# Kernel tuning notes

Hardware: AMD Instinct MI355X
Metric: run time of the kernel (lower is better)

Reference implementation:

```python
import jax, jax.numpy as jnp
import numpy as np

D_MODEL = 256
NHEAD = 8
D_FF = 2 * D_MODEL
N_LAYERS = 4
LAYER_NAMES = ("self", "cross", "self", "cross")
EPS_ATTN = 1e-6
EPS_LN = 1e-5


def pos_encoding(x):
    # LoFTR-style 2D sinusoidal positional encoding, x: [N, C, H, W]
    n, c, h, w = x.shape
    d4 = c // 4
    # exp(arange(0, c//2, 2) * (-log(1e4) / (c//2)))
    div = jnp.exp(jnp.arange(d4, dtype=jnp.float32) * 2.0 * (-np.log(10000.0) / (c // 2)))
    xs = jnp.arange(w, dtype=jnp.float32)[None, None, :]   # [1,1,W]
    ys = jnp.arange(h, dtype=jnp.float32)[None, :, None]   # [1,H,1]
    dv = div[:, None, None]                                 # [d4,1,1]
    sx = jnp.broadcast_to(jnp.sin(xs * dv), (d4, h, w))
    cx = jnp.broadcast_to(jnp.cos(xs * dv), (d4, h, w))
    sy = jnp.broadcast_to(jnp.sin(ys * dv), (d4, h, w))
    cy = jnp.broadcast_to(jnp.cos(ys * dv), (d4, h, w))
    pe = jnp.stack([sx, cx, sy, cy], axis=1).reshape(c, h, w)  # channel order pe[0::4]=sin_x,...
    return x + pe[None]


def linear_attention(q, k, v):
    # q: [N,L,H,d], k/v: [N,S,H,d]
    Q = jax.nn.elu(q) + 1.0
    K = jax.nn.elu(k) + 1.0
    KV = jnp.einsum('nshd,nshm->nhmd', K, v)                 # [N,H,d,d]
    Z = 1.0 / (jnp.einsum('nlhd,nhd->nlh', Q, K.sum(axis=1)) + EPS_ATTN)
    return jnp.einsum('nlhd,nhmd,nlh->nlhm', Q, KV, Z)       # [N,L,H,d]


def layer_norm(x, g, b):
    m = jnp.mean(x, axis=-1, keepdims=True)
    v = jnp.mean(jnp.square(x - m), axis=-1, keepdims=True)
    return (x - m) / jnp.sqrt(v + EPS_LN) * g + b


def encoder_layer(x, src, p):
    N, L, _ = x.shape
    q = (x @ p['Wq'] + p['bq']).reshape(N, L, NHEAD, -1)
    S = src.shape[1]
    k = (src @ p['Wk'] + p['bk']).reshape(N, S, NHEAD, -1)
    v = (src @ p['Wv'] + p['bv']).reshape(N, S, NHEAD, -1)
    attn = linear_attention(q, k, v).reshape(N, L, -1) @ p['Wo'] + p['bo']
    x = layer_norm(x + attn, p['g1'], p['be1'])
    y = jax.nn.relu(x @ p['W1'] + p['b1']) @ p['W2'] + p['b2']
    return layer_norm(x + y, p['g2'], p['be2'])


def _params_at(i, Wq, bq, Wk, bk, Wv, bv, Wo, bo, W1, b1, W2, b2, g1, be1, g2, be2):
    return dict(Wq=Wq[i], bq=bq[i], Wk=Wk[i], bk=bk[i], Wv=Wv[i], bv=bv[i],
                Wo=Wo[i], bo=bo[i], W1=W1[i], b1=b1[i], W2=W2[i], b2=b2[i],
                g1=g1[i], be1=be1[i], g2=g2[i], be2=be2[i])


def setup_inputs() -> dict:
    key = jax.random.key(0)
    ks = jax.random.split(key, 16)
    N, C, H, W = 4, D_MODEL, 64, 64
    d, dff, Ln = D_MODEL, D_FF, N_LAYERS
    s = 1.0 / np.sqrt(d)
    sf = 1.0 / np.sqrt(dff)
    return {
        'ref_feature': jax.random.normal(ks[0], (N, C, H, W), jnp.float32),
        'src_feature': jax.random.normal(ks[1], (N, C, H, W), jnp.float32),
        'Wq': jax.random.normal(ks[2], (Ln, d, d), jnp.float32) * s,
        'bq': jnp.zeros((Ln, d), jnp.float32),
        'Wk': jax.random.normal(ks[3], (Ln, d, d), jnp.float32) * s,
        'bk': jnp.zeros((Ln, d), jnp.float32),
        'Wv': jax.random.normal(ks[4], (Ln, d, d), jnp.float32) * s,
        'bv': jnp.zeros((Ln, d), jnp.float32),
        'Wo': jax.random.normal(ks[5], (Ln, d, d), jnp.float32) * s,
        'bo': jnp.zeros((Ln, d), jnp.float32),
        'W1': jax.random.normal(ks[6], (Ln, d, dff), jnp.float32) * s,
        'b1': jnp.zeros((Ln, dff), jnp.float32),
        'W2': jax.random.normal(ks[7], (Ln, dff, d), jnp.float32) * sf,
        'b2': jnp.zeros((Ln, d), jnp.float32),
        'g1': jnp.ones((Ln, d), jnp.float32),
        'be1': jnp.zeros((Ln, d), jnp.float32),
        'g2': jnp.ones((Ln, d), jnp.float32),
        'be2': jnp.zeros((Ln, d), jnp.float32),
    }


def reference(ref_feature, src_feature, Wq, bq, Wk, bk, Wv, bv, Wo, bo,
              W1, b1, W2, b2, g1, be1, g2, be2):
    # FMT.forward(feat='cross')
    N, C, H, W = ref_feature.shape
    f0 = pos_encoding(ref_feature).transpose(0, 2, 3, 1).reshape(N, H * W, C)
    f1 = pos_encoding(src_feature).transpose(0, 2, 3, 1).reshape(N, H * W, C)
    p1 = jnp.concatenate([f0, f1], axis=0)   # [2N, L, C]
    p2 = jnp.concatenate([f1, f0], axis=0)
    for i, name in enumerate(LAYER_NAMES):
        p = _params_at(i, Wq, bq, Wk, bk, Wv, bv, Wo, bo, W1, b1, W2, b2, g1, be1, g2, be2)
        src = p1 if name == 'self' else p2
        p1 = encoder_layer(p1, src, p)
    out = p1.reshape(2 * N, H, W, C).transpose(0, 3, 1, 2)  # [2N, C, H, W]
    return out
```

## Files before the change

kernel.cpp:

```cpp
#include <hip/hip_runtime.h>
#include <hip/hip_bf16.h>

typedef __bf16 bf16;
typedef __attribute__((ext_vector_type(8))) __bf16 bf16x8;
typedef __attribute__((ext_vector_type(4))) __bf16 bf16x4;
typedef __attribute__((ext_vector_type(4))) float f32x4;

__device__ __forceinline__ bf16 f2bf(float f) { return (bf16)f; }

__device__ __forceinline__ void async_cp16(const void* g, void* l) {
    __builtin_amdgcn_global_load_lds(
        (const __attribute__((address_space(1))) unsigned int*)g,
        (__attribute__((address_space(3))) unsigned int*)l, 16, 0, 0);
}

__device__ __forceinline__ float pe_val(int c, int t) {
    int h = t >> 6, w = t & 63;
    int i = c >> 2, j = c & 3;
    float div = expf(-0.14391156831212787f * (float)i);
    float arg = ((j < 2) ? (float)w : (float)h) * div;
    return (j & 1) ? cosf(arg) : sinf(arg);
}

__global__ __launch_bounds__(1024) void encode_kernel(const float* __restrict__ ref,
                                                      const float* __restrict__ src,
                                                      bf16* __restrict__ Xb,
                                                      bf16* __restrict__ P2b) {
    __shared__ float tile[32][33];
    int n = blockIdx.z >> 1, sel = blockIdx.z & 1;
    const float* f = sel ? src : ref;
    int t = blockIdx.x * 32 + threadIdx.x;
    int c = blockIdx.y * 32 + threadIdx.y;
    float v = f[((size_t)n * 256 + c) * 4096 + t] + pe_val(c, t);
    tile[threadIdx.y][threadIdx.x] = v;
    __syncthreads();
    int tt = blockIdx.x * 32 + threadIdx.y;
    int cc = blockIdx.y * 32 + threadIdx.x;
    float o = tile[threadIdx.x][threadIdx.y];
    int bx = sel ? 4 + n : n;
    int bp = sel ? n : 4 + n;
    Xb [((size_t)bx * 4096 + tt) * 256 + cc] = f2bf(o);
    P2b[((size_t)bp * 4096 + tt) * 256 + cc] = f2bf(o);
}

__global__ __launch_bounds__(1024) void wt_conv(const float* __restrict__ Wq, const float* __restrict__ Wk,
                                                const float* __restrict__ Wv, const float* __restrict__ Wo,
                                                const float* __restrict__ W1, const float* __restrict__ W2,
                                                bf16* __restrict__ Wt) {
    __shared__ float t[32][33];
    int z = blockIdx.z, L = z / 6, m = z - L * 6;
    const float* src; int K, N, doff;
    if      (m == 0) { src = Wq + L * 65536;  K = 256; N = 256; doff = 0; }
    else if (m == 1) { src = Wk + L * 65536;  K = 256; N = 256; doff = 65536; }
    else if (m == 2) { src = Wv + L * 65536;  K = 256; N = 256; doff = 131072; }
    else if (m == 3) { src = Wo + L * 65536;  K = 256; N = 256; doff = 196608; }
    else if (m == 4) { src = W1 + L * 131072; K = 256; N = 512; doff = 262144; }
    else             { src = W2 + L * 131072; K = 512; N = 256; doff = 393216; }
    int n0 = blockIdx.x * 32, k0 = blockIdx.y * 32;
    if (n0 >= N || k0 >= K) return;
    t[threadIdx.y][threadIdx.x] = src[(size_t)(k0 + threadIdx.y) * N + n0 + threadIdx.x];
    __syncthreads();
    bf16* dst = Wt + (size_t)L * 524288 + doff;
    dst[(size_t)(n0 + threadIdx.y) * K + k0 + threadIdx.x] = f2bf(t[threadIdx.x][threadIdx.y]);
}

__global__ __launch_bounds__(256) void gemm_qkv(const bf16* __restrict__ Aq,
                                                const bf16* __restrict__ Akv,
                                                const bf16* __restrict__ Wt,
                                                const float* __restrict__ bq,
                                                const float* __restrict__ bk,
                                                const float* __restrict__ bv,
                                                bf16* __restrict__ Q,
                                                bf16* __restrict__ Ko,
                                                bf16* __restrict__ V) {
    __shared__ bf16 Als[128 * 64];
    __shared__ bf16 Bls[128 * 64];
    int tid = threadIdx.x;
    int wave = tid >> 6, lane = tid & 63;
    int bm = blockIdx.y * 128, bn = blockIdx.x * 128;
    int wm = (wave >> 1) * 64, wn = (wave & 1) * 64;
    int l15 = lane & 15, g = lane >> 4;
    const int K = 256;

    int seg = bn >> 8, cloc = bn & 255;
    const bf16* A = seg == 0 ? Aq : Akv;
    const float* bias = seg == 0 ? bq : (seg == 1 ? bk : bv);
    bf16* Out = seg == 0 ? Q : (seg == 1 ? Ko : V);
    bool do_elu = seg < 2;

    f32x4 acc[4][4] = {};

    for (int k0 = 0; k0 < K; k0 += 64) {
#pragma unroll
        for (int r = 0; r < 4; ++r) {
            int Lc = r * 256 + tid;
            int row = Lc >> 3, cs = Lc & 7;
            int gc = cs ^ (row & 7);
            async_cp16(A  + (size_t)(bm + row) * K + k0 + gc * 8, &Als[Lc * 8]);
            async_cp16(Wt + (size_t)(bn + row) * K + k0 + gc * 8, &Bls[Lc * 8]);
        }
        __syncthreads();
#pragma unroll
        for (int ks = 0; ks < 2; ++ks) {
            bf16x8 af[4], bfr[4];
#pragma unroll
            for (int i = 0; i < 4; ++i) {
                int row = wm + i * 16 + l15;
                int c = ks * 4 + g;
                af[i] = *(bf16x8*)&Als[row * 64 + ((c ^ (row & 7)) * 8)];
            }
#pragma unroll
            for (int j = 0; j < 4; ++j) {
                int row = wn + j * 16 + l15;
                int c = ks * 4 + g;
                bfr[j] = *(bf16x8*)&Bls[row * 64 + ((c ^ (row & 7)) * 8)];
            }
#pragma unroll
            for (int i = 0; i < 4; ++i)
#pragma unroll
                for (int j = 0; j < 4; ++j)
                    acc[i][j] = __builtin_amdgcn_mfma_f32_16x16x32_bf16(af[i], bfr[j], acc[i][j], 0, 0, 0);
        }
        __syncthreads();
    }

    int r4 = (lane >> 4) * 4;
#pragma unroll
    for (int i = 0; i < 4; ++i) {
#pragma unroll
        for (int j = 0; j < 4; ++j) {
            int cj = cloc + wn + j * 16 + l15;
            float bvv = bias[cj];
#pragma unroll
            for (int r = 0; r < 4; ++r) {
                int row = bm + wm + i * 16 + r4 + r;
                float v = acc[i][j][r] + bvv;
                if (do_elu) v = v > 0.f ? v + 1.f : expf(v);
                Out[(size_t)row * 256 + cj] = f2bf(v);
            }
        }
    }
}

template <int RELU>
__global__ __launch_bounds__(256) void gemm_mfma(const bf16* __restrict__ A,
                                                 const bf16* __restrict__ Wt,
                                                 const float* __restrict__ bias,
                                                 bf16* __restrict__ C,
                                                 int N, int K) {
    __shared__ bf16 Als[128 * 64];
    __shared__ bf16 Bls[128 * 64];
    int tid = threadIdx.x;
    int wave = tid >> 6, lane = tid & 63;
    int bm = blockIdx.y * 128, bn = blockIdx.x * 128;
    int wm = (wave >> 1) * 64, wn = (wave & 1) * 64;
    int l15 = lane & 15, g = lane >> 4;

    f32x4 acc[4][4] = {};

    for (int k0 = 0; k0 < K; k0 += 64) {
#pragma unroll
        for (int r = 0; r < 4; ++r) {
            int Lc = r * 256 + tid;
            int row = Lc >> 3, cs = Lc & 7;
            int gc = cs ^ (row & 7);
            async_cp16(A  + (size_t)(bm + row) * K + k0 + gc * 8, &Als[Lc * 8]);
            async_cp16(Wt + (size_t)(bn + row) * K + k0 + gc * 8, &Bls[Lc * 8]);
        }
        __syncthreads();
#pragma unroll
        for (int ks = 0; ks < 2; ++ks) {
            bf16x8 af[4], bfr[4];
#pragma unroll
            for (int i = 0; i < 4; ++i) {
                int row = wm + i * 16 + l15;
                int c = ks * 4 + g;
                af[i] = *(bf16x8*)&Als[row * 64 + ((c ^ (row & 7)) * 8)];
            }
#pragma unroll
            for (int j = 0; j < 4; ++j) {
                int row = wn + j * 16 + l15;
                int c = ks * 4 + g;
                bfr[j] = *(bf16x8*)&Bls[row * 64 + ((c ^ (row & 7)) * 8)];
            }
#pragma unroll
            for (int i = 0; i < 4; ++i)
#pragma unroll
                for (int j = 0; j < 4; ++j)
                    acc[i][j] = __builtin_amdgcn_mfma_f32_16x16x32_bf16(af[i], bfr[j], acc[i][j], 0, 0, 0);
        }
        __syncthreads();
    }

    int r4 = (lane >> 4) * 4;
#pragma unroll
    for (int i = 0; i < 4; ++i) {
#pragma unroll
        for (int j = 0; j < 4; ++j) {
            int col = bn + wn + j * 16 + l15;
            float bvv = bias[col];
#pragma unroll
            for (int r = 0; r < 4; ++r) {
                int row = bm + wm + i * 16 + r4 + r;
                float v = acc[i][j][r] + bvv;
                if (RELU) v = fmaxf(v, 0.f);
                C[(size_t)row * N + col] = f2bf(v);
            }
        }
    }
}

__global__ __launch_bounds__(512) void gemm_ln(const bf16* __restrict__ A,
                                               const bf16* __restrict__ Wt,
                                               const float* __restrict__ bias,
                                               bf16* __restrict__ Xb,
                                               const float* __restrict__ g,
                                               const float* __restrict__ b,
                                               int K) {
    __shared__ __align__(16) char smem[128 * 260 * 2];
    bf16* Als = (bf16*)smem;
    bf16* Bls = (bf16*)(smem + 16384);
    bf16* Cls = (bf16*)smem;

    int tid = threadIdx.x;
    int wave = tid >> 6, lane = tid & 63;
    int bm = blockIdx.x * 128;
    int wm = (wave >> 2) * 64, wn = (wave & 3) * 64;
    int l15 = lane & 15, gg = lane >> 4;

    f32x4 acc[4][4] = {};

    for (int k0 = 0; k0 < K; k0 += 64) {
#pragma unroll
        for (int r = 0; r < 2; ++r) {
            int Lc = r * 512 + tid;
            int row = Lc >> 3, cs = Lc & 7;
            int gc = cs ^ (row & 7);
            async_cp16(A + (size_t)(bm + row) * K + k0 + gc * 8, &Als[Lc * 8]);
        }
#pragma unroll
        for (int r = 0; r < 4; ++r) {
            int Lc = r * 512 + tid;
            int row = Lc >> 3, cs = Lc & 7;
            int gc = cs ^ (row & 7);
            async_cp16(Wt + (size_t)row * K + k0 + gc * 8, &Bls[Lc * 8]);
        }
        __syncthreads();
#pragma unroll
        for (int ks = 0; ks < 2; ++ks) {
            bf16x8 af[4], bfr[4];
#pragma unroll
            for (int i = 0; i < 4; ++i) {
                int row = wm + i * 16 + l15;
                int c = ks * 4 + gg;
                af[i] = *(bf16x8*)&Als[row * 64 + ((c ^ (row & 7)) * 8)];
            }
#pragma unroll
            for (int j = 0; j < 4; ++j) {
                int row = wn + j * 16 + l15;
                int c = ks * 4 + gg;
                bfr[j] = *(bf16x8*)&Bls[row * 64 + ((c ^ (row & 7)) * 8)];
            }
#pragma unroll
            for (int i = 0; i < 4; ++i)
#pragma unroll
                for (int j = 0; j < 4; ++j)
                    acc[i][j] = __builtin_amdgcn_mfma_f32_16x16x32_bf16(af[i], bfr[j], acc[i][j], 0, 0, 0);
        }
        __syncthreads();
    }

    int r4 = (lane >> 4) * 4;
#pragma unroll
    for (int j = 0; j < 4; ++j) {
        int col = wn + j * 16 + l15;
        float bvv = bias[col];
#pragma unroll
        for (int i = 0; i < 4; ++i)
#pragma unroll
            for (int r = 0; r < 4; ++r)
                Cls[(wm + i * 16 + r4 + r) * 260 + col] = f2bf(acc[i][j][r] + bvv);
    }
    __syncthreads();

    int c4 = lane * 4;
    float4 gw = *(const float4*)&g[c4];
    float4 bw = *(const float4*)&b[c4];
#pragma unroll 2
    for (int rw = 0; rw < 16; ++rw) {
        int row = wave * 16 + rw;
        size_t gidx = (size_t)(bm + row) * 256 + c4;
        bf16x4 xb = *(const bf16x4*)(Xb + gidx);
        bf16x4 cb = *(const bf16x4*)&Cls[row * 260 + c4];
        float4 v;
        v.x = (float)xb[0] + (float)cb[0];
        v.y = (float)xb[1] + (float)cb[1];
        v.z = (float)xb[2] + (float)cb[2];
        v.w = (float)xb[3] + (float)cb[3];
        float s  = v.x + v.y + v.z + v.w;
        float sq = v.x * v.x + v.y * v.y + v.z * v.z + v.w * v.w;
#pragma unroll
        for (int off = 32; off > 0; off >>= 1) {
            s  += __shfl_xor(s,  off);
            sq += __shfl_xor(sq, off);
        }
        float mean = s * (1.f / 256.f);
        float var  = sq * (1.f / 256.f) - mean * mean;
        float rstd = rsqrtf(var + 1e-5f);
        bf16x4 ob;
        ob[0] = f2bf((v.x - mean) * rstd * gw.x + bw.x);
        ob[1] = f2bf((v.y - mean) * rstd * gw.y + bw.y);
        ob[2] = f2bf((v.z - mean) * rstd * gw.z + bw.z);
        ob[3] = f2bf((v.w - mean) * rstd * gw.w + bw.w);
        *(bf16x4*)(Xb + gidx) = ob;
    }
}

__global__ __launch_bounds__(256) void kv_prep_part(const bf16* __restrict__ Kb,
                                                    const bf16* __restrict__ Vb,
                                                    float* __restrict__ Pkv,
                                                    float* __restrict__ Pks) {
    __shared__ float Ks[128][32];
    __shared__ float Vs[128][32];
    int sp = blockIdx.x;
    int nh = blockIdx.y;
    int n = nh >> 3, h = nh & 7;
    int tid = threadIdx.x;
    int wave = tid >> 6, lane = tid & 63;
    int mg = lane >> 3;
    int dg = lane & 7;
    size_t base = ((size_t)n * 4096 + sp * 128) * 256 + h * 32;

#pragma unroll
    for (int p = 0; p < 2; ++p) {
        int r = p * 64 + (tid >> 2);
        int c = (tid & 3) * 8;
        bf16x8 k8 = *(const bf16x8*)(Kb + base + (size_t)r * 256 + c);
        bf16x8 v8 = *(const bf16x8*)(Vb + base + (size_t)r * 256 + c);
#pragma unroll
        for (int u = 0; u < 8; ++u) { Ks[r][c + u] = (float)k8[u]; Vs[r][c + u] = (float)v8[u]; }
    }
    __syncthreads();

    float acc[4][4] = {};
    float ks4[4] = {};
    int s0 = wave * 32;
    for (int s = s0; s < s0 + 32; ++s) {
        float4 kq = *(float4*)&Ks[s][dg * 4];
        float4 vq = *(float4*)&Vs[s][mg * 4];
        ks4[0] += kq.x; ks4[1] += kq.y; ks4[2] += kq.z; ks4[3] += kq.w;
        acc[0][0] += vq.x * kq.x; acc[0][1] += vq.x * kq.y; acc[0][2] += vq.x * kq.z; acc[0][3] += vq.x * kq.w;
        acc[1][0] += vq.y * kq.x; acc[1][1] += vq.y * kq.y; acc[1][2] += vq.y * kq.z; acc[1][3] += vq.y * kq.w;
        acc[2][0] += vq.z * kq.x; acc[2][1] += vq.z * kq.y; acc[2][2] += vq.z * kq.z; acc[2][3] += vq.z * kq.w;
        acc[3][0] += vq.w * kq.x; acc[3][1] += vq.w * kq.y; acc[3][2] += vq.w * kq.z; acc[3][3] += vq.w * kq.w;
    }
    __syncthreads();

    float* R  = &Ks[0][0];
    float* RS = &Vs[0][0];
#pragma unroll
    for (int mi = 0; mi < 4; ++mi)
#pragma unroll
        for (int dj = 0; dj < 4; ++dj)
            R[wave * 1024 + (mg * 4 + mi) * 32 + dg * 4 + dj] = acc[mi][dj];
    if (mg == 0)
#pragma unroll
        for (int dj = 0; dj < 4; ++dj) RS[wave * 32 + dg * 4 + dj] = ks4[dj];
    __syncthreads();

    int e = tid * 4;
    float4 o0 = *(float4*)&R[e];
    float4 o1 = *(float4*)&R[1024 + e];
    float4 o2 = *(float4*)&R[2048 + e];
    float4 o3 = *(float4*)&R[3072 + e];
    float4 o = make_float4(o0.x + o1.x + o2.x + o3.x, o0.y + o1.y + o2.y + o3.y,
                           o0.z + o1.z + o2.z + o3.z, o0.w + o1.w + o2.w + o3.w);
    *(float4*)&Pkv[((size_t)nh * 32 + sp) * 1024 + e] = o;
    if (tid < 32)
        Pks[((size_t)nh * 32 + sp) * 32 + tid] = RS[tid] + RS[32 + tid] + RS[64 + tid] + RS[96 + tid];
}

__global__ __launch_bounds__(64) void kv_reduce(const float* __restrict__ Pkv,
                                                const float* __restrict__ Pks,
                                                float* __restrict__ KV,
                                                float* __restrict__ Ksum) {
    int nh = blockIdx.x;
    int q = blockIdx.y;
    int e = (q * 64 + threadIdx.x) * 4;
    float4 s = make_float4(0.f, 0.f, 0.f, 0.f);
    for (int sp = 0; sp < 32; ++sp) {
        float4 p = *(const float4*)&Pkv[((size_t)nh * 32 + sp) * 1024 + e];
        s.x += p.x; s.y += p.y; s.z += p.z; s.w += p.w;
    }
    *(float4*)&KV[(size_t)nh * 1024 + e] = s;
    if (q == 0 && threadIdx.x < 32) {
        float ss = 0.f;
        for (int sp = 0; sp < 32; ++sp) ss += Pks[((size_t)nh * 32 + sp) * 32 + threadIdx.x];
        Ksum[nh * 32 + threadIdx.x] = ss;
    }
}

__global__ __launch_bounds__(256) void attn_apply(const bf16* __restrict__ Qb,
                                                  const float* __restrict__ KV,
                                                  const float* __restrict__ Ksum,
                                                  bf16* __restrict__ B) {
    __shared__ float Qs[32][260];
    __shared__ float Zs[32][8];
    int bx = blockIdx.x;
    int n = bx >> 7;
    int tok0 = (bx & 127) << 5;
    int tid = threadIdx.x;

    const bf16* qsrc = Qb + ((size_t)(n * 4096 + tok0)) * 256;
#pragma unroll
    for (int kk = 0; kk < 4; ++kk) {
        int e8 = tid + kk * 256;
        bf16x8 v = *(const bf16x8*)(qsrc + (size_t)e8 * 8);
        int t = e8 >> 5, c8 = e8 & 31;
#pragma unroll
        for (int u = 0; u < 8; ++u) Qs[t][c8 * 8 + u] = (float)v[u];
    }

    int h = tid >> 5, m = tid & 31;
    float kvr[32];
    const float* kvp = KV + (size_t)(n * 8 + h) * 1024 + m * 32;
#pragma unroll
    for (int c = 0; c < 8; ++c) *(float4*)&kvr[c * 4] = *(const float4*)(kvp + c * 4);
    __syncthreads();

    {
        int tz = tid >> 3, hz = tid & 7;
        const float* ksp = Ksum + n * 256 + hz * 32;
        float z = 0.f;
#pragma unroll
        for (int c = 0; c < 8; ++c) {
            float4 q = *(float4*)&Qs[tz][hz * 32 + c * 4];
            float4 k = *(const float4*)(ksp + c * 4);
            z += q.x * k.x + q.y * k.y + q.z * k.z + q.w * k.w;
        }
        Zs[tz][hz] = 1.f / (z + 1e-6f);
    }
    __syncthreads();

    bf16* outp = B + ((size_t)(n * 4096 + tok0)) * 256 + tid;
#pragma unroll 2
    for (int t = 0; t < 32; ++t) {
        float acc = 0.f;
#pragma unroll
        for (int c = 0; c < 8; ++c) {
            float4 q = *(float4*)&Qs[t][h * 32 + c * 4];
            acc += q.x * kvr[c * 4 + 0] + q.y * kvr[c * 4 + 1]
                 + q.z * kvr[c * 4 + 2] + q.w * kvr[c * 4 + 3];
        }
        outp[(size_t)t * 256] = f2bf(acc * Zs[t][h]);
    }
}

__global__ __launch_bounds__(1024) void store_kernel(const bf16* __restrict__ Xb,
                                                     float* __restrict__ out) {
    __shared__ float tile[32][33];
    int b = blockIdx.z;
    int t0 = blockIdx.x * 32, c0 = blockIdx.y * 32;
    tile[threadIdx.y][threadIdx.x] =
        (float)Xb[((size_t)b * 4096 + t0 + threadIdx.y) * 256 + c0 + threadIdx.x];
    __syncthreads();
    out[((size_t)b * 256 + c0 + threadIdx.y) * 4096 + t0 + threadIdx.x] =
        tile[threadIdx.x][threadIdx.y];
}

extern "C" void kernel_launch(void* const* d_in, const int* in_sizes, int n_in,
                              void* d_out, int out_size, void* d_ws, size_t ws_size,
                              hipStream_t stream) {
    const float* ref  = (const float*)d_in[0];
    const float* srcf = (const float*)d_in[1];
    const float* Wq = (const float*)d_in[2];
    const float* bq = (const float*)d_in[3];
    const float* Wk = (const float*)d_in[4];
    const float* bk = (const float*)d_in[5];
    const float* Wv = (const float*)d_in[6];
    const float* bv = (const float*)d_in[7];
    const float* Wo = (const float*)d_in[8];
    const float* bo = (const float*)d_in[9];
    const float* W1 = (const float*)d_in[10];
    const float* b1 = (const float*)d_in[11];
    const float* W2 = (const float*)d_in[12];
    const float* b2 = (const float*)d_in[13];
    const float* g1 = (const float*)d_in[14];
    const float* be1 = (const float*)d_in[15];
    const float* g2 = (const float*)d_in[16];
    const float* be2 = (const float*)d_in[17];

    const size_t SZ = (size_t)8 * 4096 * 256;
    float* ws  = (float*)d_ws;
    float* KVb = ws;
    float* Ksb = KVb + 65536;
    float* Pkv = Ksb + 2048;
    float* Pks = Pkv + 2097152;
    bf16*  Wt  = (bf16*)(Pks + 65536);
    bf16*  Xb  = Wt + 2097152;
    bf16*  P2b = Xb + SZ;
    bf16*  Qb  = P2b + SZ;
    bf16*  Kb  = (bf16*)d_out;
    bf16*  Vb  = Kb + SZ;
    bf16*  Bb  = Kb;
    bf16*  Hb  = Kb;

    wt_conv<<<dim3(16, 16, 24), dim3(32, 32), 0, stream>>>(Wq, Wk, Wv, Wo, W1, W2, Wt);
    encode_kernel<<<dim3(128, 8, 8), dim3(32, 32), 0, stream>>>(ref, srcf, Xb, P2b);

    for (int L = 0; L < 4; ++L) {
        const bf16* WtL = Wt + (size_t)L * 524288;
        const bf16* Akv = (L & 1) ? P2b : Xb;
        gemm_qkv<<<dim3(6, 256), 256, 0, stream>>>(Xb, Akv, WtL,
                                                   bq + L * 256, bk + L * 256, bv + L * 256,
                                                   Qb, Kb, Vb);
        kv_prep_part<<<dim3(32, 64), 256, 0, stream>>>(Kb, Vb, Pkv, Pks);
        kv_reduce<<<dim3(64, 4), 64, 0, stream>>>(Pkv, Pks, KVb, Ksb);
        attn_apply<<<1024, 256, 0, stream>>>(Qb, KVb, Ksb, Bb);
        gemm_ln<<<256, 512, 0, stream>>>(Bb, WtL + 196608, bo + L * 256, Xb,
                                         g1 + L * 256, be1 + L * 256, 256);
        gemm_mfma<1><<<dim3(4, 256), 256, 0, stream>>>(Xb, WtL + 262144, b1 + L * 512, Hb, 512, 256);
        gemm_ln<<<256, 512, 0, stream>>>(Hb, WtL + 393216, b2 + L * 256, Xb,
                                         g2 + L * 256, be2 + L * 256, 512);
    }

    store_kernel<<<dim3(128, 8, 8), dim3(32, 32), 0, stream>>>(Xb, (float*)d_out);
}
```

Measured before the change: 691.0 us.

## Fuse attention apply with output projection and LayerNorm into one kernel

Replaces the separate attn_apply kernel and the following gemm_ln (Wo projection + residual + LayerNorm) with a single kernel that computes the attention output for 128 rows into swizzled shared memory and then runs the MFMA projection and LayerNorm from it. This removes the global write and re-read of the attention output buffer and one kernel launch per layer. In exchange, each block uses about 130 KB of LDS and runs the attention phase serially in four 32-token chunks, with only 256 blocks, which lowers occupancy and parallelism for that phase.

```diff
diff --git a/kernel.cpp b/kernel.cpp
--- a/kernel.cpp
+++ b/kernel.cpp
@@ -316,6 +316,161 @@
     }
 }
 
+__global__ __launch_bounds__(512) void attn_oln(const bf16* __restrict__ Qb,
+                                                const float* __restrict__ KV,
+                                                const float* __restrict__ Ksum,
+                                                const bf16* __restrict__ Wt,
+                                                const float* __restrict__ bias,
+                                                bf16* __restrict__ Xb,
+                                                const float* __restrict__ g,
+                                                const float* __restrict__ b) {
+    __shared__ __align__(16) char smem[132096];
+    __shared__ float Zs[32][8];
+    float* Qs  = (float*)smem;
+    bf16*  Wls = (bf16*)smem;
+    bf16*  Cls = (bf16*)smem;
+    bf16*  Bt  = (bf16*)(smem + 66560);
+
+    int tid = threadIdx.x;
+    int r0 = blockIdx.x * 128;
+    int n = r0 >> 12;
+
+    int c = tid & 255, tg = tid >> 8;
+    int h = c >> 5, m = c & 31;
+    float kvr[32];
+    const float* kvp = KV + (size_t)(n * 8 + h) * 1024 + m * 32;
+#pragma unroll
+    for (int q4 = 0; q4 < 8; ++q4) *(float4*)&kvr[q4 * 4] = *(const float4*)(kvp + q4 * 4);
+
+    int col8 = (c >> 3) & 7, elem = c & 7, slice = c >> 6;
+
+    for (int it = 0; it < 4; ++it) {
+        int t0 = it * 32;
+        const bf16* qsrc = Qb + (size_t)(r0 + t0) * 256;
+#pragma unroll
+        for (int kk = 0; kk < 2; ++kk) {
+            int e8 = kk * 512 + tid;
+            bf16x8 v = *(const bf16x8*)(qsrc + (size_t)e8 * 8);
+            int t = e8 >> 5, c8 = e8 & 31;
+#pragma unroll
+            for (int u = 0; u < 8; ++u) Qs[t * 260 + c8 * 8 + u] = (float)v[u];
+        }
+        __syncthreads();
+        if (tid < 256) {
+            int tz = tid >> 3, hz = tid & 7;
+            const float* ksp = Ksum + n * 256 + hz * 32;
+            float z = 0.f;
+#pragma unroll
+            for (int q4 = 0; q4 < 8; ++q4) {
+                float4 qv = *(float4*)&Qs[tz * 260 + hz * 32 + q4 * 4];
+                float4 kq = *(const float4*)(ksp + q4 * 4);
+                z += qv.x * kq.x + qv.y * kq.y + qv.z * kq.z + qv.w * kq.w;
+            }
+            Zs[tz][hz] = 1.f / (z + 1e-6f);
+        }
+        __syncthreads();
+#pragma unroll 2
+        for (int tt = 0; tt < 16; ++tt) {
+            int t = tg * 16 + tt;
+            float acc = 0.f;
+#pragma unroll
+            for (int q4 = 0; q4 < 8; ++q4) {
+                float4 qv = *(float4*)&Qs[t * 260 + h * 32 + q4 * 4];
+                acc += qv.x * kvr[q4 * 4 + 0] + qv.y * kvr[q4 * 4 + 1]
+                     + qv.z * kvr[q4 * 4 + 2] + qv.w * kvr[q4 * 4 + 3];
+            }
+            int row = t0 + t;
+            Bt[slice * 8192 + row * 64 + ((col8 ^ (row & 7)) * 8) + elem] =
+                f2bf(acc * Zs[t][h]);
+        }
+        __syncthreads();
+    }
+
+    int wave = tid >> 6, lane = tid & 63;
+    int wm = (wave >> 2) * 64, wn = (wave & 3) * 64;
+    int l15 = lane & 15, gg = lane >> 4;
+    f32x4 acc[4][4] = {};
+
+    for (int k0 = 0; k0 < 256; k0 += 64) {
+#pragma unroll
+        for (int r = 0; r < 4; ++r) {
+            int Lc = r * 512 + tid;
+            int row = Lc >> 3, cs = Lc & 7;
+            int gc = cs ^ (row & 7);
+            async_cp16(Wt + (size_t)row * 256 + k0 + gc * 8, &Wls[Lc * 8]);
+        }
+        __syncthreads();
+        const bf16* Asl = Bt + (k0 >> 6) * 8192;
+#pragma unroll
+        for (int ks = 0; ks < 2; ++ks) {
+            bf16x8 af[4], bfr[4];
+#pragma unroll
+            for (int i = 0; i < 4; ++i) {
+                int row = wm + i * 16 + l15;
+                int cc = ks * 4 + gg;
+                af[i] = *(bf16x8*)&Asl[row * 64 + ((cc ^ (row & 7)) * 8)];
+            }
+#pragma unroll
+            for (int j = 0; j < 4; ++j) {
+                int row = wn + j * 16 + l15;
+                int cc = ks * 4 + gg;
+                bfr[j] = *(bf16x8*)&Wls[row * 64 + ((cc ^ (row & 7)) * 8)];
+            }
+#pragma unroll
+            for (int i = 0; i < 4; ++i)
+#pragma unroll
+                for (int j = 0; j < 4; ++j)
+                    acc[i][j] = __builtin_amdgcn_mfma_f32_16x16x32_bf16(af[i], bfr[j], acc[i][j], 0, 0, 0);
+        }
+        __syncthreads();
+    }
+
+    int r4 = (lane >> 4) * 4;
+#pragma unroll
+    for (int j = 0; j < 4; ++j) {
+        int col = wn + j * 16 + l15;
+        float bvv = bias[col];
+#pragma unroll
+        for (int i = 0; i < 4; ++i)
+#pragma unroll
+            for (int r = 0; r < 4; ++r)
+                Cls[(wm + i * 16 + r4 + r) * 260 + col] = f2bf(acc[i][j][r] + bvv);
+    }
+    __syncthreads();
+
+    int c4 = lane * 4;
+    float4 gw = *(const float4*)&g[c4];
+    float4 bw = *(const float4*)&b[c4];
+#pragma unroll 2
+    for (int rw = 0; rw < 16; ++rw) {
+        int row = wave * 16 + rw;
+        size_t gidx = (size_t)(r0 + row) * 256 + c4;
+        bf16x4 xb = *(const bf16x4*)(Xb + gidx);
+        bf16x4 cb = *(const bf16x4*)&Cls[row * 260 + c4];
+        float4 v;
+        v.x = (float)xb[0] + (float)cb[0];
+        v.y = (float)xb[1] + (float)cb[1];
+        v.z = (float)xb[2] + (float)cb[2];
+        v.w = (float)xb[3] + (float)cb[3];
+        float s  = v.x + v.y + v.z + v.w;
+        float sq = v.x * v.x + v.y * v.y + v.z * v.z + v.w * v.w;
+#pragma unroll
+        for (int off = 32; off > 0; off >>= 1) {
+            s  += __shfl_xor(s,  off);
+            sq += __shfl_xor(sq, off);
+        }
+        float mean = s * (1.f / 256.f);
+        float var  = sq * (1.f / 256.f) - mean * mean;
+        float rstd = rsqrtf(var + 1e-5f);
+        bf16x4 ob;
+        ob[0] = f2bf((v.x - mean) * rstd * gw.x + bw.x);
+        ob[1] = f2bf((v.y - mean) * rstd * gw.y + bw.y);
+        ob[2] = f2bf((v.z - mean) * rstd * gw.z + bw.z);
+        ob[3] = f2bf((v.w - mean) * rstd * gw.w + bw.w);
+        *(bf16x4*)(Xb + gidx) = ob;
+    }
+}
+
 __global__ __launch_bounds__(256) void kv_prep_part(const bf16* __restrict__ Kb,
                                                     const bf16* __restrict__ Vb,
                                                     float* __restrict__ Pkv,
@@ -397,62 +552,6 @@
         float ss = 0.f;
         for (int sp = 0; sp < 32; ++sp) ss += Pks[((size_t)nh * 32 + sp) * 32 + threadIdx.x];
         Ksum[nh * 32 + threadIdx.x] = ss;
-    }
-}
-
-__global__ __launch_bounds__(256) void attn_apply(const bf16* __restrict__ Qb,
-                                                  const float* __restrict__ KV,
-                                                  const float* __restrict__ Ksum,
-                                                  bf16* __restrict__ B) {
-    __shared__ float Qs[32][260];
-    __shared__ float Zs[32][8];
-    int bx = blockIdx.x;
-    int n = bx >> 7;
-    int tok0 = (bx & 127) << 5;
-    int tid = threadIdx.x;
-
-    const bf16* qsrc = Qb + ((size_t)(n * 4096 + tok0)) * 256;
-#pragma unroll
-    for (int kk = 0; kk < 4; ++kk) {
-        int e8 = tid + kk * 256;
-        bf16x8 v = *(const bf16x8*)(qsrc + (size_t)e8 * 8);
-        int t = e8 >> 5, c8 = e8 & 31;
-#pragma unroll
-        for (int u = 0; u < 8; ++u) Qs[t][c8 * 8 + u] = (float)v[u];
-    }
-
-    int h = tid >> 5, m = tid & 31;
-    float kvr[32];
-    const float* kvp = KV + (size_t)(n * 8 + h) * 1024 + m * 32;
-#pragma unroll
-    for (int c = 0; c < 8; ++c) *(float4*)&kvr[c * 4] = *(const float4*)(kvp + c * 4);
-    __syncthreads();
-
-    {
-        int tz = tid >> 3, hz = tid & 7;
-        const float* ksp = Ksum + n * 256 + hz * 32;
-        float z = 0.f;
-#pragma unroll
-        for (int c = 0; c < 8; ++c) {
-            float4 q = *(float4*)&Qs[tz][hz * 32 + c * 4];
-            float4 k = *(const float4*)(ksp + c * 4);
-            z += q.x * k.x + q.y * k.y + q.z * k.z + q.w * k.w;
-        }
-        Zs[tz][hz] = 1.f / (z + 1e-6f);
-    }
-    __syncthreads();
-
-    bf16* outp = B + ((size_t)(n * 4096 + tok0)) * 256 + tid;
-#pragma unroll 2
-    for (int t = 0; t < 32; ++t) {
-        float acc = 0.f;
-#pragma unroll
-        for (int c = 0; c < 8; ++c) {
-            float4 q = *(float4*)&Qs[t][h * 32 + c * 4];
-            acc += q.x * kvr[c * 4 + 0] + q.y * kvr[c * 4 + 1]
-                 + q.z * kvr[c * 4 + 2] + q.w * kvr[c * 4 + 3];
-        }
-        outp[(size_t)t * 256] = f2bf(acc * Zs[t][h]);
     }
 }
 
@@ -502,7 +601,6 @@
     bf16*  Qb  = P2b + SZ;
     bf16*  Kb  = (bf16*)d_out;
     bf16*  Vb  = Kb + SZ;
-    bf16*  Bb  = Kb;
     bf16*  Hb  = Kb;
 
     wt_conv<<<dim3(16, 16, 24), dim3(32, 32), 0, stream>>>(Wq, Wk, Wv, Wo, W1, W2, Wt);
@@ -516,9 +614,8 @@
                                                    Qb, Kb, Vb);
         kv_prep_part<<<dim3(32, 64), 256, 0, stream>>>(Kb, Vb, Pkv, Pks);
         kv_reduce<<<dim3(64, 4), 64, 0, stream>>>(Pkv, Pks, KVb, Ksb);
-        attn_apply<<<1024, 256, 0, stream>>>(Qb, KVb, Ksb, Bb);
-        gemm_ln<<<256, 512, 0, stream>>>(Bb, WtL + 196608, bo + L * 256, Xb,
-                                         g1 + L * 256, be1 + L * 256, 256);
+        attn_oln<<<256, 512, 0, stream>>>(Qb, KVb, Ksb, WtL + 196608, bo + L * 256,
+                                          Xb, g1 + L * 256, be1 + L * 256);
         gemm_mfma<1><<<dim3(4, 256), 256, 0, stream>>>(Xb, WtL + 262144, b1 + L * 512, Hb, 512, 256);
         gemm_ln<<<256, 512, 0, stream>>>(Hb, WtL + 393216, b2 + L * 256, Xb,
                                          g2 + L * 256, be2 + L * 256, 512);
```

Measured after the change: 673.9 us. 1.03x faster.

## Fold KV into output projection weights and stage GEMM epilogues through LDS

Applied to the files above, without the earlier changes.

Drops the attention-apply pass by folding each batch's per-head KV matrix into the output projection. This builds a per-batch effective weight Weff = Wo·blockdiag(KV). Q is then scaled in place by its normaliser Z, and the LN GEMM uses the per-batch weights directly, which removes one full activation read/write pass. The qkv and FFN GEMM epilogues also now stage results in shared memory so they can write coalesced 16-byte rows. The cost is an extra small weff kernel, a separate zscale pass over Q, bf16 rounding of the fused weights, and extra LDS use.

```diff
diff --git a/kernel.cpp b/kernel.cpp
--- a/kernel.cpp
+++ b/kernel.cpp
@@ -73,8 +73,10 @@
                                                 bf16* __restrict__ Q,
                                                 bf16* __restrict__ Ko,
                                                 bf16* __restrict__ V) {
-    __shared__ bf16 Als[128 * 64];
-    __shared__ bf16 Bls[128 * 64];
+    __shared__ __align__(16) char qsm[128 * 140 * 2];
+    bf16* Als = (bf16*)qsm;
+    bf16* Bls = (bf16*)(qsm + 16384);
+    bf16* Cls = (bf16*)qsm;
     int tid = threadIdx.x;
     int wave = tid >> 6, lane = tid & 63;
     int bm = blockIdx.y * 128, bn = blockIdx.x * 128;
@@ -129,17 +131,23 @@
     for (int i = 0; i < 4; ++i) {
 #pragma unroll
         for (int j = 0; j < 4; ++j) {
-            int cj = cloc + wn + j * 16 + l15;
-            float bvv = bias[cj];
+            int col = wn + j * 16 + l15;
+            float bvv = bias[cloc + col];
 #pragma unroll
             for (int r = 0; r < 4; ++r) {
-                int row = bm + wm + i * 16 + r4 + r;
                 float v = acc[i][j][r] + bvv;
                 if (do_elu) v = v > 0.f ? v + 1.f : expf(v);
-                Out[(size_t)row * 256 + cj] = f2bf(v);
-            }
-        }
-    }
+                Cls[(wm + i * 16 + r4 + r) * 140 + col] = f2bf(v);
+            }
+        }
+    }
+    __syncthreads();
+    int row = tid >> 1, half = tid & 1;
+    const bf16* srcr = Cls + row * 140 + half * 64;
+    bf16* dstr = Out + (size_t)(bm + row) * 256 + cloc + half * 64;
+#pragma unroll
+    for (int u = 0; u < 8; ++u)
+        *(bf16x8*)(dstr + u * 8) = *(const bf16x8*)(srcr + u * 8);
 }
 
 template <int RELU>
@@ -148,8 +156,10 @@
                                                  const float* __restrict__ bias,
                                                  bf16* __restrict__ C,
                                                  int N, int K) {
-    __shared__ bf16 Als[128 * 64];
-    __shared__ bf16 Bls[128 * 64];
+    __shared__ __align__(16) char qsm[128 * 140 * 2];
+    bf16* Als = (bf16*)qsm;
+    bf16* Bls = (bf16*)(qsm + 16384);
+    bf16* Cls = (bf16*)qsm;
     int tid = threadIdx.x;
     int wave = tid >> 6, lane = tid & 63;
     int bm = blockIdx.y * 128, bn = blockIdx.x * 128;
@@ -197,26 +207,32 @@
     for (int i = 0; i < 4; ++i) {
 #pragma unroll
         for (int j = 0; j < 4; ++j) {
-            int col = bn + wn + j * 16 + l15;
-            float bvv = bias[col];
+            int col = wn + j * 16 + l15;
+            float bvv = bias[bn + col];
 #pragma unroll
             for (int r = 0; r < 4; ++r) {
-                int row = bm + wm + i * 16 + r4 + r;
                 float v = acc[i][j][r] + bvv;
                 if (RELU) v = fmaxf(v, 0.f);
-                C[(size_t)row * N + col] = f2bf(v);
-            }
-        }
-    }
-}
-
-__global__ __launch_bounds__(512) void gemm_ln(const bf16* __restrict__ A,
-                                               const bf16* __restrict__ Wt,
-                                               const float* __restrict__ bias,
-                                               bf16* __restrict__ Xb,
-                                               const float* __restrict__ g,
-                                               const float* __restrict__ b,
-                                               int K) {
+                Cls[(wm + i * 16 + r4 + r) * 140 + col] = f2bf(v);
+            }
+        }
+    }
+    __syncthreads();
+    int row = tid >> 1, half = tid & 1;
+    const bf16* srcr = Cls + row * 140 + half * 64;
+    bf16* dstr = C + (size_t)(bm + row) * N + bn + half * 64;
+#pragma unroll
+    for (int u = 0; u < 8; ++u)
+        *(bf16x8*)(dstr + u * 8) = *(const bf16x8*)(srcr + u * 8);
+}
+
+__global__ __launch_bounds__(512) void gemm_lnW(const bf16* __restrict__ A,
+                                                const bf16* __restrict__ Wt,
+                                                const float* __restrict__ bias,
+                                                bf16* __restrict__ Xb,
+                                                const float* __restrict__ g,
+                                                const float* __restrict__ b,
+                                                int K, int per_batch) {
     __shared__ __align__(16) char smem[128 * 260 * 2];
     bf16* Als = (bf16*)smem;
     bf16* Bls = (bf16*)(smem + 16384);
@@ -225,6 +241,7 @@
     int tid = threadIdx.x;
     int wave = tid >> 6, lane = tid & 63;
     int bm = blockIdx.x * 128;
+    if (per_batch) Wt += (size_t)(bm >> 12) * 65536;
     int wm = (wave >> 2) * 64, wn = (wave & 3) * 64;
     int l15 = lane & 15, gg = lane >> 4;
 
@@ -400,60 +417,72 @@
     }
 }
 
-__global__ __launch_bounds__(256) void attn_apply(const bf16* __restrict__ Qb,
-                                                  const float* __restrict__ KV,
-                                                  const float* __restrict__ Ksum,
-                                                  bf16* __restrict__ B) {
-    __shared__ float Qs[32][260];
-    __shared__ float Zs[32][8];
-    int bx = blockIdx.x;
-    int n = bx >> 7;
-    int tok0 = (bx & 127) << 5;
+__global__ __launch_bounds__(256) void weff_kernel(const float* __restrict__ KV,
+                                                   const bf16* __restrict__ WtO,
+                                                   bf16* __restrict__ Weff) {
+    __shared__ float KVs[8][1024];
+    int n = blockIdx.y, c0 = blockIdx.x * 64;
     int tid = threadIdx.x;
-
-    const bf16* qsrc = Qb + ((size_t)(n * 4096 + tok0)) * 256;
-#pragma unroll
-    for (int kk = 0; kk < 4; ++kk) {
-        int e8 = tid + kk * 256;
-        bf16x8 v = *(const bf16x8*)(qsrc + (size_t)e8 * 8);
-        int t = e8 >> 5, c8 = e8 & 31;
-#pragma unroll
-        for (int u = 0; u < 8; ++u) Qs[t][c8 * 8 + u] = (float)v[u];
-    }
-
-    int h = tid >> 5, m = tid & 31;
-    float kvr[32];
-    const float* kvp = KV + (size_t)(n * 8 + h) * 1024 + m * 32;
-#pragma unroll
-    for (int c = 0; c < 8; ++c) *(float4*)&kvr[c * 4] = *(const float4*)(kvp + c * 4);
-    __syncthreads();
-
-    {
-        int tz = tid >> 3, hz = tid & 7;
-        const float* ksp = Ksum + n * 256 + hz * 32;
-        float z = 0.f;
-#pragma unroll
-        for (int c = 0; c < 8; ++c) {
-            float4 q = *(float4*)&Qs[tz][hz * 32 + c * 4];
-            float4 k = *(const float4*)(ksp + c * 4);
-            z += q.x * k.x + q.y * k.y + q.z * k.z + q.w * k.w;
-        }
-        Zs[tz][hz] = 1.f / (z + 1e-6f);
-    }
-    __syncthreads();
-
-    bf16* outp = B + ((size_t)(n * 4096 + tok0)) * 256 + tid;
-#pragma unroll 2
-    for (int t = 0; t < 32; ++t) {
-        float acc = 0.f;
-#pragma unroll
-        for (int c = 0; c < 8; ++c) {
-            float4 q = *(float4*)&Qs[t][h * 32 + c * 4];
-            acc += q.x * kvr[c * 4 + 0] + q.y * kvr[c * 4 + 1]
-                 + q.z * kvr[c * 4 + 2] + q.w * kvr[c * 4 + 3];
-        }
-        outp[(size_t)t * 256] = f2bf(acc * Zs[t][h]);
-    }
+    const float* src = KV + (size_t)n * 8192;
+    for (int i = tid; i < 2048; i += 256)
+        *(float4*)&((float*)KVs)[i * 4] = *(const float4*)&src[i * 4];
+    __syncthreads();
+
+    int c = c0 + (tid & 63);
+    int hb = tid >> 6;
+    const bf16* wrow = WtO + (size_t)c * 256 + hb * 64;
+    bf16* dst = Weff + (size_t)n * 65536 + (size_t)c * 256 + hb * 64;
+
+#pragma unroll
+    for (int hh = 0; hh < 2; ++hh) {
+        int h = hb * 2 + hh;
+        float wo[32];
+#pragma unroll
+        for (int u = 0; u < 4; ++u) {
+            bf16x8 w8 = *(const bf16x8*)(wrow + hh * 32 + u * 8);
+#pragma unroll
+            for (int v = 0; v < 8; ++v) wo[u * 8 + v] = (float)w8[v];
+        }
+        float s[32] = {};
+        for (int m = 0; m < 32; ++m) {
+            float wm = wo[m];
+#pragma unroll
+            for (int d4 = 0; d4 < 8; ++d4) {
+                float4 kv4 = *(float4*)&KVs[h][m * 32 + d4 * 4];
+                s[d4 * 4 + 0] += wm * kv4.x;
+                s[d4 * 4 + 1] += wm * kv4.y;
+                s[d4 * 4 + 2] += wm * kv4.z;
+                s[d4 * 4 + 3] += wm * kv4.w;
+            }
+        }
+#pragma unroll
+        for (int u = 0; u < 4; ++u) {
+            bf16x8 o8;
+#pragma unroll
+            for (int v = 0; v < 8; ++v) o8[v] = f2bf(s[u * 8 + v]);
+            *(bf16x8*)(dst + hh * 32 + u * 8) = o8;
+        }
+    }
+}
+
+__global__ __launch_bounds__(256) void zscale(bf16* __restrict__ Qb,
+                                              const float* __restrict__ Ksum) {
+    int row = blockIdx.x * 4 + (threadIdx.x >> 6);
+    int lane = threadIdx.x & 63;
+    int n = row >> 12;
+    int c = lane * 4;
+    bf16* p = Qb + (size_t)row * 256 + c;
+    bf16x4 q = *(const bf16x4*)p;
+    float4 k = *(const float4*)&Ksum[n * 256 + c];
+    float s = (float)q[0] * k.x + (float)q[1] * k.y + (float)q[2] * k.z + (float)q[3] * k.w;
+    s += __shfl_xor(s, 1); s += __shfl_xor(s, 2); s += __shfl_xor(s, 4);
+    float z = 1.f / (s + 1e-6f);
+    bf16x4 o;
+    o[0] = f2bf((float)q[0] * z);
+    o[1] = f2bf((float)q[1] * z);
+    o[2] = f2bf((float)q[2] * z);
+    o[3] = f2bf((float)q[3] * z);
+    *(bf16x4*)p = o;
 }
 
 __global__ __launch_bounds__(1024) void store_kernel(const bf16* __restrict__ Xb,
@@ -500,9 +529,9 @@
     bf16*  Xb  = Wt + 2097152;
     bf16*  P2b = Xb + SZ;
     bf16*  Qb  = P2b + SZ;
+    bf16*  Weffb = (bf16*)Pkv;
     bf16*  Kb  = (bf16*)d_out;
     bf16*  Vb  = Kb + SZ;
-    bf16*  Bb  = Kb;
     bf16*  Hb  = Kb;
 
     wt_conv<<<dim3(16, 16, 24), dim3(32, 32), 0, stream>>>(Wq, Wk, Wv, Wo, W1, W2, Wt);
@@ -516,12 +545,13 @@
                                                    Qb, Kb, Vb);
         kv_prep_part<<<dim3(32, 64), 256, 0, stream>>>(Kb, Vb, Pkv, Pks);
         kv_reduce<<<dim3(64, 4), 64, 0, stream>>>(Pkv, Pks, KVb, Ksb);
-        attn_apply<<<1024, 256, 0, stream>>>(Qb, KVb, Ksb, Bb);
-        gemm_ln<<<256, 512, 0, stream>>>(Bb, WtL + 196608, bo + L * 256, Xb,
-                                         g1 + L * 256, be1 + L * 256, 256);
+        weff_kernel<<<dim3(4, 8), 256, 0, stream>>>(KVb, WtL + 196608, Weffb);
+        zscale<<<8192, 256, 0, stream>>>(Qb, Ksb);
+        gemm_lnW<<<256, 512, 0, stream>>>(Qb, Weffb, bo + L * 256, Xb,
+                                          g1 + L * 256, be1 + L * 256, 256, 1);
         gemm_mfma<1><<<dim3(4, 256), 256, 0, stream>>>(Xb, WtL + 262144, b1 + L * 512, Hb, 512, 256);
-        gemm_ln<<<256, 512, 0, stream>>>(Hb, WtL + 393216, b2 + L * 256, Xb,
-                                         g2 + L * 256, be2 + L * 256, 512);
+        gemm_lnW<<<256, 512, 0, stream>>>(Hb, WtL + 393216, b2 + L * 256, Xb,
+                                          g2 + L * 256, be2 + L * 256, 512, 0);
     }
 
     store_kernel<<<dim3(128, 8, 8), dim3(32, 32), 0, stream>>>(Xb, (float*)d_out);
```

Result: slower. 745.2 us (+7.9%).
